# Performance work log

Measured on AMD Instinct MI355X. Metric: run time of the kernel, lower is better.

The kernel has to match this reference:

```python
import jax, jax.numpy as jnp
import numpy as np

V = 32000   # vocab_size
E = 512     # embedding_size
H = 512     # hidden_size
B = 32      # batch
T = 48      # caption seq_len
BOS = 1     # bos token id


def _xavier(key, shape):
    fan_out, fan_in = shape
    lim = np.sqrt(6.0 / (fan_in + fan_out)).astype(np.float32)
    return jax.random.uniform(key, shape, jnp.float32, -lim, lim)


def setup_inputs() -> dict:
    key = jax.random.key(0)
    ks = jax.random.split(key, 6)
    return {
        "image_features": jax.random.normal(ks[0], (1, B, E), jnp.float32),
        "ground_truth_captions": jax.random.randint(ks[1], (B, T), 0, V),
        "embedding": _xavier(ks[2], (V, E)),
        "W_ih": _xavier(ks[3], (4 * H, E)),
        "W_hh": _xavier(ks[4], (4 * H, H)),
        "b_ih": jnp.zeros((4 * H,), jnp.float32),
        "b_hh": jnp.zeros((4 * H,), jnp.float32),
        "W_head": _xavier(ks[5], (V, H)),
        "b_head": jnp.zeros((V,), jnp.float32),
    }


def _lstm_step(carry, x, W_ih, W_hh, b):
    # PyTorch LSTM cell: gate order i, f, g, o
    h, c = carry
    gates = x @ W_ih.T + h @ W_hh.T + b          # [B, 4H]
    i, f, g, o = jnp.split(gates, 4, axis=-1)
    c = jax.nn.sigmoid(f) * c + jax.nn.sigmoid(i) * jnp.tanh(g)
    h = jax.nn.sigmoid(o) * jnp.tanh(c)
    return (h, c), h


def reference(image_features, ground_truth_captions, embedding,
              W_ih, W_hh, b_ih, b_hh, W_head, b_head):
    b = b_ih + b_hh
    bsz = image_features.shape[1]
    step = lambda carry, x: _lstm_step(carry, x, W_ih, W_hh, b)

    # _init_step: run LSTM over image features from zero state
    h0 = jnp.zeros((bsz, H), image_features.dtype)
    c0 = jnp.zeros((bsz, H), image_features.dtype)
    (h, c), _ = jax.lax.scan(step, (h0, c0), image_features)

    # teacher-forced input tokens for steps t = 1 .. T-1:
    # [bos, gt[:,1], ..., gt[:,T-2]]  -> shape [T-1, B]
    tokens = jnp.concatenate(
        [jnp.full((1, bsz), BOS, ground_truth_captions.dtype),
         ground_truth_captions[:, 1:T - 1].T], axis=0)
    emb = embedding[tokens]                      # [T-1, B, E]

    (_, _), hs = jax.lax.scan(step, (h, c), emb)  # [T-1, B, H]
    logits = jnp.einsum('tbh,vh->tbv', hs, W_head) + b_head  # [T-1, B, V]

    # outputs[0] stays zero, as in the torch loop
    outputs = jnp.concatenate(
        [jnp.zeros((1, bsz, V), logits.dtype), logits], axis=0)
    return outputs
```

## Files before the change

kernel.cpp:

```cpp
#include <hip/hip_runtime.h>
#include <hip/hip_bf16.h>

#define V_ 32000
#define E_ 512
#define H_ 512
#define B_ 32
#define T_ 48
#define NWG 16
#define NCON 125
#define GRID (NWG + 1 + NCON)
#define SPIN_CAP (1 << 20)

typedef __attribute__((ext_vector_type(8))) short bf16x8;
typedef __attribute__((ext_vector_type(4))) float f32x4;
typedef __attribute__((ext_vector_type(4))) int   i32x4;
typedef __attribute__((ext_vector_type(2))) int   i32x2;

static __device__ __forceinline__ short f2bf(float f) {
  union { __hip_bfloat16 h; short s; } u;
  u.h = __float2bfloat16(f);
  return u.s;
}

static __device__ __forceinline__ bf16x8 load_cvt8(const float* p) {
  float4 a = *(const float4*)p;
  float4 b = *(const float4*)(p + 4);
  bf16x8 r;
  r[0] = f2bf(a.x); r[1] = f2bf(a.y); r[2] = f2bf(a.z); r[3] = f2bf(a.w);
  r[4] = f2bf(b.x); r[5] = f2bf(b.y); r[6] = f2bf(b.z); r[7] = f2bf(b.w);
  return r;
}

static __device__ __forceinline__ float sigf(float x) {
  return 1.0f / (1.0f + __expf(-x));
}
static __device__ __forceinline__ float tanh_fast(float x) {
  float e = __expf(2.0f * x);
  return (e - 1.0f) / (e + 1.0f);
}

static __device__ __forceinline__ unsigned prog_load(const unsigned* p) {
  unsigned v;
  asm volatile("global_load_dword %0, %1, off sc0 sc1\n\t"
               "s_waitcnt vmcnt(0)"
               : "=&v"(v) : "v"(p) : "memory");
  return v;
}

#define DSTORE(ADDR, VAL)                                              \
  asm volatile("global_store_dword %0, %1, off sc0 sc1"                \
               :: "v"(ADDR), "v"(VAL) : "memory")
#define DSTORE2(ADDR, VAL)                                             \
  asm volatile("global_store_dwordx2 %0, %1, off sc0 sc1"              \
               :: "v"(ADDR), "v"(VAL) : "memory")

__global__ __launch_bounds__(256) void k_xg(
    const float* __restrict__ img,
    const int*   __restrict__ gt,
    const float* __restrict__ emb,
    const float* __restrict__ W_ih,
    const float* __restrict__ b_ih,
    const float* __restrict__ b_hh,
    float* __restrict__ Xg)
{
  const int s    = blockIdx.x;
  const int lane = threadIdx.x & 63;
  const int wv   = threadIdx.x >> 6;
  const int nbase = blockIdx.y * 256 + wv * 64;
  const int lr  = lane & 15;
  const int lkb = lane >> 4;

  const float* arow[2];
#pragma unroll
  for (int m = 0; m < 2; ++m) {
    int b = m * 16 + lr;
    const float* src;
    if (s == 0) {
      src = img + b * E_;
    } else {
      int tok = (s == 1) ? 1 : gt[b * T_ + (s - 1)];
      src = emb + (long)tok * E_;
    }
    arow[m] = src;
  }

  f32x4 acc[2][4];
#pragma unroll
  for (int m = 0; m < 2; ++m)
#pragma unroll
    for (int n = 0; n < 4; ++n) acc[m][n] = (f32x4){0.f, 0.f, 0.f, 0.f};

  for (int kt = 0; kt < 16; ++kt) {
    int ko = kt * 32 + lkb * 8;
    bf16x8 a0 = load_cvt8(arow[0] + ko);
    bf16x8 a1 = load_cvt8(arow[1] + ko);
#pragma unroll
    for (int n = 0; n < 4; ++n) {
      const float* wp = W_ih + (long)(nbase + n * 16 + lr) * E_ + ko;
      bf16x8 bw = load_cvt8(wp);
      acc[0][n] = __builtin_amdgcn_mfma_f32_16x16x32_bf16(a0, bw, acc[0][n], 0, 0, 0);
      acc[1][n] = __builtin_amdgcn_mfma_f32_16x16x32_bf16(a1, bw, acc[1][n], 0, 0, 0);
    }
  }

#pragma unroll
  for (int n = 0; n < 4; ++n) {
    int j = nbase + n * 16 + lr;
    float bias = b_ih[j] + b_hh[j];
#pragma unroll
    for (int m = 0; m < 2; ++m) {
#pragma unroll
      for (int r = 0; r < 4; ++r) {
        int b = m * 16 + lkb * 4 + r;
        Xg[((long)(s * B_ + b) * 2048) + j] = acc[m][n][r] + bias;
      }
    }
  }
}

__global__ __launch_bounds__(256, 1) void k_fused(
    const float* __restrict__ W_hh,
    const float* __restrict__ Xg,
    const float* __restrict__ W_head,
    const float* __restrict__ b_head,
    unsigned* __restrict__ flags,
    unsigned* __restrict__ replicas,
    unsigned short* __restrict__ hrot,
    unsigned short* __restrict__ hs,
    float* __restrict__ out)
{
  __shared__ __align__(16) char lds[147456];
  const int tid  = threadIdx.x;
  const int lane = tid & 63;
  const int wv   = tid >> 6;
  const int lr   = lane & 15;
  const int lkb  = lane >> 4;

  __builtin_amdgcn_fence(__ATOMIC_ACQUIRE, "agent");

  if (blockIdx.x < NWG) {
    char* wlds  = lds;
    char* stage = lds + 98304;
    char* gbufc = lds + 131072;
    const int w = blockIdx.x;
    const int g = wv;

    bf16x8 awr[2][4];
#pragma unroll
    for (int rt = 0; rt < 2; ++rt) {
      int row = g * 512 + w * 32 + rt * 16 + lr;
#pragma unroll
      for (int kt = 0; kt < 12; ++kt) {
        bf16x8 wf = load_cvt8(W_hh + (long)row * E_ + kt * 32 + lkb * 8);
        *(bf16x8*)(wlds + ((((wv * 2 + rt) * 12 + kt) * 64) + lane) * 16) = wf;
      }
#pragma unroll
      for (int kt = 12; kt < 16; ++kt)
        awr[rt][kt - 12] = load_cvt8(W_hh + (long)row * E_ + kt * 32 + lkb * 8);
    }

    const int cb_b  = tid >> 3;
    const int cb_di = (tid & 7) * 4;
    f32x4 cst = (f32x4){0.f, 0.f, 0.f, 0.f};
    __syncthreads();

    for (int t = 0; t < T_; ++t) {
      float4 xg[2][2];
#pragma unroll
      for (int rt = 0; rt < 2; ++rt)
#pragma unroll
        for (int bt = 0; bt < 2; ++bt)
          xg[rt][bt] = *(const float4*)(Xg + ((long)t * B_ + bt * 16 + lr) * 2048 +
                                        g * 512 + w * 32 + rt * 16 + lkb * 4);

      f32x4 acc[2][2];
#pragma unroll
      for (int rt = 0; rt < 2; ++rt) {
        acc[rt][0] = (f32x4){0.f, 0.f, 0.f, 0.f};
        acc[rt][1] = (f32x4){0.f, 0.f, 0.f, 0.f};
      }

      if (t > 0) {
        if (wv == 0) {
          for (int it = 0; it < SPIN_CAP; ++it) {
            unsigned v = 0xFFFFFFFFu;
            if (lane < NWG) v = prog_load(flags + lane * 32);
            if (__ballot(v >= (unsigned)t) == ~0ULL) break;
            __builtin_amdgcn_s_sleep(1);
          }
        }
        __syncthreads();

        const i32x4* src = (const i32x4*)((const char*)hrot +
                                          (long)(t - 1) * 32768 + tid * 128);
        i32x4 u[8];
#pragma unroll
        for (int c = 0; c < 8; ++c) u[c] = src[c];

        int b_own = tid >> 3, j0b = (tid & 7) * 128;
#pragma unroll
        for (int c = 0; c < 8; ++c)
          *(i32x4*)(stage + b_own * 1024 + ((j0b + c * 16) ^ ((b_own & 7) << 4))) = u[c];
        __syncthreads();

#pragma unroll
        for (int kt = 0; kt < 16; ++kt) {
          int b0r = lr, b1r = 16 + lr;
          i32x4 bv0 = *(const i32x4*)(stage + b0r * 1024 +
                                      ((kt * 64 + lkb * 16) ^ ((b0r & 7) << 4)));
          i32x4 bv1 = *(const i32x4*)(stage + b1r * 1024 +
                                      ((kt * 64 + lkb * 16) ^ ((b1r & 7) << 4)));
          bf16x8 b0 = *(bf16x8*)&bv0, b1 = *(bf16x8*)&bv1;
#pragma unroll
          for (int rt = 0; rt < 2; ++rt) {
            bf16x8 a;
            if (kt < 12) a = *(const bf16x8*)(wlds +
                             ((((wv * 2 + rt) * 12 + kt) * 64) + lane) * 16);
            else a = awr[rt][kt - 12];
            acc[rt][0] = __builtin_amdgcn_mfma_f32_16x16x32_bf16(a, b0, acc[rt][0], 0, 0, 0);
            acc[rt][1] = __builtin_amdgcn_mfma_f32_16x16x32_bf16(a, b1, acc[rt][1], 0, 0, 0);
          }
        }
      }

#pragma unroll
      for (int rt = 0; rt < 2; ++rt)
#pragma unroll
        for (int bt = 0; bt < 2; ++bt) {
          int b = bt * 16 + lr;
          f32x4 r = acc[rt][bt];
          r[0] += xg[rt][bt].x; r[1] += xg[rt][bt].y;
          r[2] += xg[rt][bt].z; r[3] += xg[rt][bt].w;
          *(f32x4*)(gbufc + (g * 32 + b) * 128 +
                    (((rt * 16 + lkb * 4) * 4) ^ ((b & 7) << 4))) = r;
        }
      __syncthreads();

      int rb = (cb_di * 4) ^ ((cb_b & 7) << 4);
      float4 gi  = *(const float4*)(gbufc + (0 * 32 + cb_b) * 128 + rb);
      float4 gf  = *(const float4*)(gbufc + (1 * 32 + cb_b) * 128 + rb);
      float4 gg_ = *(const float4*)(gbufc + (2 * 32 + cb_b) * 128 + rb);
      float4 go  = *(const float4*)(gbufc + (3 * 32 + cb_b) * 128 + rb);
      float iv[4] = {gi.x, gi.y, gi.z, gi.w};
      float fv[4] = {gf.x, gf.y, gf.z, gf.w};
      float gv[4] = {gg_.x, gg_.y, gg_.z, gg_.w};
      float ov[4] = {go.x, go.y, go.z, go.w};
      unsigned short hb[4];
#pragma unroll
      for (int r = 0; r < 4; ++r) {
        float c_ = sigf(fv[r]) * cst[r] + sigf(iv[r]) * tanh_fast(gv[r]);
        cst[r] = c_;
        hb[r] = (unsigned short)f2bf(sigf(ov[r]) * tanh_fast(c_));
      }
      i32x2 pk;
      pk[0] = (int)((unsigned)hb[0] | ((unsigned)hb[1] << 16));
      pk[1] = (int)((unsigned)hb[2] | ((unsigned)hb[3] << 16));

      if (t < T_ - 1) {
        unsigned short* hn = hrot + (long)t * (B_ * H_) + cb_b * H_ + w * 32 + cb_di;
        DSTORE2(hn, pk);
      }
      if (t >= 1) {
        unsigned short* hp = hs + ((long)(t - 1) * B_ + cb_b) * H_ + w * 32 + cb_di;
        DSTORE2(hp, pk);
      }
      asm volatile("s_waitcnt vmcnt(0)" ::: "memory");
      __syncthreads();
      if (tid == 0) DSTORE(flags + w * 32, (unsigned)(t + 1));
    }
  } else if (blockIdx.x == NWG) {
    if (tid < 64) {
      for (unsigned e = 2; e <= (unsigned)T_; ++e) {
        for (int it = 0; it < SPIN_CAP; ++it) {
          unsigned f = (lane < NWG) ? prog_load(flags + lane * 32) : 0xFFFFFFFFu;
          if (__ballot(f >= e) == ~0ULL) break;
          __builtin_amdgcn_s_sleep(2);
        }
        DSTORE(replicas + lane * 32, e);
      }
    }
  } else {
    char* stage = lds;
    const int cid = blockIdx.x - NWG - 1;

    bf16x8 bw[4][16];
    float bias[4];
#pragma unroll
    for (int j = 0; j < 4; ++j) {
      int v = cid * 256 + j * 64 + wv * 16 + lr;
#pragma unroll
      for (int kt = 0; kt < 16; ++kt)
        bw[j][kt] = load_cvt8(W_head + (long)v * E_ + kt * 32 + lkb * 8);
      bias[j] = b_head[v];
    }

    for (int mt = 0; mt < 94; ++mt) {
      int tagneed = mt / 2 + 2;
      if (tid == 0) {
        const unsigned* rp = replicas + (cid & 63) * 32;
        for (int it = 0; it < SPIN_CAP; ++it) {
          if (prog_load(rp) >= (unsigned)tagneed) break;
          __builtin_amdgcn_s_sleep(32);
        }
      }
      __syncthreads();

      const i32x4* src = (const i32x4*)((const char*)(hs + (long)mt * 16 * H_) + tid * 64);
      i32x4 st[4];
#pragma unroll
      for (int i = 0; i < 4; ++i) st[i] = src[i];
#pragma unroll
      for (int i = 0; i < 4; ++i) {
        int c = tid * 4 + i;
        int row = c >> 6;
        int cb  = (c & 63) * 16;
        *(i32x4*)(stage + row * 1024 + (cb ^ ((row & 7) << 4))) = st[i];
      }
      __syncthreads();

      f32x4 acc[4];
#pragma unroll
      for (int j = 0; j < 4; ++j)
        acc[j] = (f32x4){bias[j], bias[j], bias[j], bias[j]};
#pragma unroll
      for (int kt = 0; kt < 16; ++kt) {
        int cb = kt * 64 + lkb * 16;
        i32x4 av = *(const i32x4*)(stage + lr * 1024 + (cb ^ ((lr & 7) << 4)));
        bf16x8 a = *(bf16x8*)&av;
#pragma unroll
        for (int j = 0; j < 4; ++j)
          acc[j] = __builtin_amdgcn_mfma_f32_16x16x32_bf16(a, bw[j][kt], acc[j], 0, 0, 0);
      }

#pragma unroll
      for (int j = 0; j < 4; ++j)
#pragma unroll
        for (int r = 0; r < 4; ++r) {
          int R = mt * 16 + lkb * 4 + r;
          out[(long)(R + 32) * V_ + cid * 256 + j * 64 + wv * 16 + lr] = acc[j][r];
        }
    }
  }
}

extern "C" void kernel_launch(void* const* d_in, const int* in_sizes, int n_in,
                              void* d_out, int out_size, void* d_ws, size_t ws_size,
                              hipStream_t stream) {
  const float* img  = (const float*)d_in[0];
  const int*   gt   = (const int*)d_in[1];
  const float* emb  = (const float*)d_in[2];
  const float* W_ih = (const float*)d_in[3];
  const float* W_hh = (const float*)d_in[4];
  const float* b_ih = (const float*)d_in[5];
  const float* b_hh = (const float*)d_in[6];
  const float* W_hd = (const float*)d_in[7];
  const float* b_hd = (const float*)d_in[8];
  float* out = (float*)d_out;

  char* ws = (char*)d_ws;
  unsigned*       flags = (unsigned*)(ws);
  unsigned*       repl  = (unsigned*)(ws + 8192);
  unsigned short* hrot  = (unsigned short*)(ws + 16384);
  unsigned short* hs    = (unsigned short*)(ws + 16384 + 1572864);
  float*          Xg    = (float*)(ws + 16384 + 1572864 + 1540096);

  hipMemsetAsync(ws, 0, 16384, stream);
  hipMemsetAsync(out, 0, (size_t)B_ * V_ * sizeof(float), stream);

  dim3 g1(48, 8);
  k_xg<<<g1, 256, 0, stream>>>(img, gt, emb, W_ih, b_ih, b_hh, Xg);
  k_fused<<<GRID, 256, 0, stream>>>(W_hh, Xg, W_hd, b_hd, flags, repl, hrot, hs, out);
}
```

Before: 286.2 us.

## Fuse input-gate projection into persistent kernel with per-step readiness counters

Removes the separate k_xg launch and computes the input-projection gates (x·W_ih^T + bias) inside the consumer blocks of the persistent fused kernel. Each timestep's results are published through an atomic counter, and the recurrent workgroups spin on that counter before reading the timestep's gate inputs. This removes a kernel launch boundary and lets the recurrence start as soon as the early timesteps are ready, instead of waiting for the whole projection. In exchange it adds more spin-wait synchronization and delays the consumer blocks' head-weight preload until they finish their projection work.

```diff
diff --git a/kernel.cpp b/kernel.cpp
--- a/kernel.cpp
+++ b/kernel.cpp
@@ -50,83 +50,29 @@
 #define DSTORE(ADDR, VAL)                                              \
   asm volatile("global_store_dword %0, %1, off sc0 sc1"                \
                :: "v"(ADDR), "v"(VAL) : "memory")
+#define DSTOREF(ADDR, VAL)                                             \
+  asm volatile("global_store_dword %0, %1, off sc0 sc1"                \
+               :: "v"(ADDR), "v"(VAL) : "memory")
 #define DSTORE2(ADDR, VAL)                                             \
   asm volatile("global_store_dwordx2 %0, %1, off sc0 sc1"              \
                :: "v"(ADDR), "v"(VAL) : "memory")
 
-__global__ __launch_bounds__(256) void k_xg(
+__global__ __launch_bounds__(256, 1) void k_fused(
     const float* __restrict__ img,
     const int*   __restrict__ gt,
     const float* __restrict__ emb,
     const float* __restrict__ W_ih,
     const float* __restrict__ b_ih,
     const float* __restrict__ b_hh,
-    float* __restrict__ Xg)
-{
-  const int s    = blockIdx.x;
-  const int lane = threadIdx.x & 63;
-  const int wv   = threadIdx.x >> 6;
-  const int nbase = blockIdx.y * 256 + wv * 64;
-  const int lr  = lane & 15;
-  const int lkb = lane >> 4;
-
-  const float* arow[2];
-#pragma unroll
-  for (int m = 0; m < 2; ++m) {
-    int b = m * 16 + lr;
-    const float* src;
-    if (s == 0) {
-      src = img + b * E_;
-    } else {
-      int tok = (s == 1) ? 1 : gt[b * T_ + (s - 1)];
-      src = emb + (long)tok * E_;
-    }
-    arow[m] = src;
-  }
-
-  f32x4 acc[2][4];
-#pragma unroll
-  for (int m = 0; m < 2; ++m)
-#pragma unroll
-    for (int n = 0; n < 4; ++n) acc[m][n] = (f32x4){0.f, 0.f, 0.f, 0.f};
-
-  for (int kt = 0; kt < 16; ++kt) {
-    int ko = kt * 32 + lkb * 8;
-    bf16x8 a0 = load_cvt8(arow[0] + ko);
-    bf16x8 a1 = load_cvt8(arow[1] + ko);
-#pragma unroll
-    for (int n = 0; n < 4; ++n) {
-      const float* wp = W_ih + (long)(nbase + n * 16 + lr) * E_ + ko;
-      bf16x8 bw = load_cvt8(wp);
-      acc[0][n] = __builtin_amdgcn_mfma_f32_16x16x32_bf16(a0, bw, acc[0][n], 0, 0, 0);
-      acc[1][n] = __builtin_amdgcn_mfma_f32_16x16x32_bf16(a1, bw, acc[1][n], 0, 0, 0);
-    }
-  }
-
-#pragma unroll
-  for (int n = 0; n < 4; ++n) {
-    int j = nbase + n * 16 + lr;
-    float bias = b_ih[j] + b_hh[j];
-#pragma unroll
-    for (int m = 0; m < 2; ++m) {
-#pragma unroll
-      for (int r = 0; r < 4; ++r) {
-        int b = m * 16 + lkb * 4 + r;
-        Xg[((long)(s * B_ + b) * 2048) + j] = acc[m][n][r] + bias;
-      }
-    }
-  }
-}
-
-__global__ __launch_bounds__(256, 1) void k_fused(
     const float* __restrict__ W_hh,
-    const float* __restrict__ Xg,
     const float* __restrict__ W_head,
     const float* __restrict__ b_head,
     unsigned* __restrict__ flags,
     unsigned* __restrict__ replicas,
+    unsigned* __restrict__ xgcnt,
     unsigned short* __restrict__ hrot,
     unsigned short* __restrict__ hs,
+    float* __restrict__ Xg,
     float* __restrict__ out)
 {
   __shared__ __align__(16) char lds[147456];
@@ -165,6 +111,20 @@
     __syncthreads();
 
     for (int t = 0; t < T_; ++t) {
+      if (wv == 0) {
+        for (int it = 0; it < SPIN_CAP; ++it) {
+          bool ok = true;
+          if (lane < NWG) {
+            if (t > 0) ok = (prog_load(flags + lane * 32) >= (unsigned)t);
+          } else if (lane == 16) {
+            ok = (prog_load(xgcnt + t * 32) >= 8u);
+          }
+          if (__ballot(ok) == ~0ULL) break;
+          __builtin_amdgcn_s_sleep(1);
+        }
+      }
+      __syncthreads();
+
       float4 xg[2][2];
 #pragma unroll
       for (int rt = 0; rt < 2; ++rt)
@@ -181,16 +141,6 @@
       }
 
       if (t > 0) {
-        if (wv == 0) {
-          for (int it = 0; it < SPIN_CAP; ++it) {
-            unsigned v = 0xFFFFFFFFu;
-            if (lane < NWG) v = prog_load(flags + lane * 32);
-            if (__ballot(v >= (unsigned)t) == ~0ULL) break;
-            __builtin_amdgcn_s_sleep(1);
-          }
-        }
-        __syncthreads();
-
         const i32x4* src = (const i32x4*)((const char*)hrot +
                                           (long)(t - 1) * 32768 + tid * 128);
         i32x4 u[8];
@@ -282,6 +232,65 @@
   } else {
     char* stage = lds;
     const int cid = blockIdx.x - NWG - 1;
+
+    for (int p = cid; p < 384; p += NCON) {
+      const int ts = p >> 3;
+      const int nb = (p & 7) * 256 + wv * 64;
+
+      const float* arow[2];
+#pragma unroll
+      for (int m = 0; m < 2; ++m) {
+        int b = m * 16 + lr;
+        const float* src;
+        if (ts == 0) {
+          src = img + b * E_;
+        } else {
+          int tok = (ts == 1) ? 1 : gt[b * T_ + (ts - 1)];
+          src = emb + (long)tok * E_;
+        }
+        arow[m] = src;
+      }
+
+      f32x4 acc[2][4];
+#pragma unroll
+      for (int m = 0; m < 2; ++m)
+#pragma unroll
+        for (int n = 0; n < 4; ++n) acc[m][n] = (f32x4){0.f, 0.f, 0.f, 0.f};
+
+      for (int kt = 0; kt < 16; ++kt) {
+        int ko = kt * 32 + lkb * 8;
+        bf16x8 a0 = load_cvt8(arow[0] + ko);
+        bf16x8 a1 = load_cvt8(arow[1] + ko);
+#pragma unroll
+        for (int n = 0; n < 4; ++n) {
+          const float* wp = W_ih + (long)(nb + n * 16 + lr) * E_ + ko;
+          bf16x8 bw = load_cvt8(wp);
+          acc[0][n] = __builtin_amdgcn_mfma_f32_16x16x32_bf16(a0, bw, acc[0][n], 0, 0, 0);
+          acc[1][n] = __builtin_amdgcn_mfma_f32_16x16x32_bf16(a1, bw, acc[1][n], 0, 0, 0);
+        }
+      }
+
+#pragma unroll
+      for (int n = 0; n < 4; ++n) {
+        int j = nb + n * 16 + lr;
+        float bias = b_ih[j] + b_hh[j];
+#pragma unroll
+        for (int m = 0; m < 2; ++m) {
+#pragma unroll
+          for (int r = 0; r < 4; ++r) {
+            int b = m * 16 + lkb * 4 + r;
+            float v = acc[m][n][r] + bias;
+            DSTOREF(Xg + ((long)(ts * B_ + b) * 2048) + j, v);
+          }
+        }
+      }
+      asm volatile("s_waitcnt vmcnt(0)" ::: "memory");
+      __syncthreads();
+      if (tid == 0)
+        __hip_atomic_fetch_add(xgcnt + ts * 32, 1u,
+                               __ATOMIC_RELAXED, __HIP_MEMORY_SCOPE_AGENT);
+      __syncthreads();
+    }
 
     bf16x8 bw[4][16];
     float bias[4];
@@ -360,14 +369,15 @@
   char* ws = (char*)d_ws;
   unsigned*       flags = (unsigned*)(ws);
   unsigned*       repl  = (unsigned*)(ws + 8192);
-  unsigned short* hrot  = (unsigned short*)(ws + 16384);
-  unsigned short* hs    = (unsigned short*)(ws + 16384 + 1572864);
-  float*          Xg    = (float*)(ws + 16384 + 1572864 + 1540096);
-
-  hipMemsetAsync(ws, 0, 16384, stream);
+  unsigned*       xgcnt = (unsigned*)(ws + 16384);
+  unsigned short* hrot  = (unsigned short*)(ws + 24576);
+  unsigned short* hs    = (unsigned short*)(ws + 24576 + 1572864);
+  float*          Xg    = (float*)(ws + 24576 + 1572864 + 1540096);
+
+  hipMemsetAsync(ws, 0, 24576, stream);
   hipMemsetAsync(out, 0, (size_t)B_ * V_ * sizeof(float), stream);
 
-  dim3 g1(48, 8);
-  k_xg<<<g1, 256, 0, stream>>>(img, gt, emb, W_ih, b_ih, b_hh, Xg);
-  k_fused<<<GRID, 256, 0, stream>>>(W_hh, Xg, W_hd, b_hd, flags, repl, hrot, hs, out);
-}
+  k_fused<<<GRID, 256, 0, stream>>>(img, gt, emb, W_ih, b_ih, b_hh,
+                                    W_hh, W_hd, b_hd,
+                                    flags, repl, xgcnt, hrot, hs, Xg, out);
+}
```

After: 303.4 us. 6.0% more time.
